# Optimization experiments

Hardware: AMD Instinct MI355X
Metric: run time of the kernel (lower is better)

The kernel has to match this reference:

```python
import jax, jax.numpy as jnp
import numpy as np

B, N, P, DIM, H = 8, 1024, 77, 1024, 16
HD = DIM // H
LN_EPS = 1e-5


def setup_inputs() -> dict:
    key = jax.random.key(0)
    ks = jax.random.split(key, 8)
    s = 0.02  # weight init scale
    return {
        "x": jax.random.normal(ks[0], (B, N, DIM), jnp.float32),
        "x_text": jax.random.normal(ks[1], (B, P, DIM), jnp.float32),
        "Wq": jax.random.normal(ks[2], (DIM, DIM), jnp.float32) * s,
        "Wk": jax.random.normal(ks[3], (DIM, DIM), jnp.float32) * s,
        "Wv": jax.random.normal(ks[4], (DIM, DIM), jnp.float32) * s,
        "gate": jax.random.normal(ks[5], (1, H, 1, 1), jnp.float32) * 0.5,
        "ln_g": jnp.ones((DIM,), jnp.float32),
        "ln_b": jnp.zeros((DIM,), jnp.float32),
        "Wp": jax.random.normal(ks[6], (DIM, DIM), jnp.float32) * s,
        "bp": jnp.zeros((DIM,), jnp.float32),
    }


def reference(x, x_text, Wq, Wk, Wv, gate, ln_g, ln_b, Wp, bp):
    b, n, c = x.shape
    h = gate.shape[1]
    # subln projections; prefix text tokens are concatenated onto k/v (not q)
    q = x @ Wq.T                                             # [B,N,C]
    k = jnp.concatenate([x_text @ Wk.T, x @ Wk.T], axis=1)   # [B,P+N,C]
    v = jnp.concatenate([x_text @ Wv.T, x @ Wv.T], axis=1)   # [B,P+N,C]
    kv = k.shape[1]
    q = q.reshape(b, n, h, -1).transpose(0, 2, 1, 3)         # [B,H,N,d]
    k = k.reshape(b, kv, h, -1).transpose(0, 2, 1, 3)        # [B,H,K,d]
    v = v.reshape(b, kv, h, -1).transpose(0, 2, 1, 3)        # [B,H,K,d]
    d = q.shape[-1]
    scores = jnp.einsum('bhnd,bhkd->bhnk', q, k) / jnp.sqrt(jnp.float32(d))
    # gated split softmax: first key column is softmaxed alone (== 1) and gated
    first = jnp.tanh(gate) * jnp.ones_like(scores[..., :1])  # [B,H,N,1]
    rest = jax.nn.softmax(scores[..., 1:], axis=-1)          # [B,H,N,K-1]
    attn = jnp.concatenate([first, rest], axis=-1)           # [B,H,N,K]
    out = jnp.einsum('bhnk,bhkd->bhnd', attn, v)             # AV reduce
    out = out.transpose(0, 2, 1, 3).reshape(b, n, -1)        # [B,N,C]
    # original casts to bfloat16 then back to LN weight dtype
    out = out.astype(jnp.bfloat16).astype(jnp.float32)
    mu = jnp.mean(out, axis=-1, keepdims=True)
    var = jnp.var(out, axis=-1, keepdims=True)
    out = (out - mu) / jnp.sqrt(var + LN_EPS) * ln_g + ln_b
    return out @ Wp.T + bp
```

## Files before the change

kernel.cpp:

```cpp
#include <hip/hip_runtime.h>
#include <stdint.h>

#define DIM   1024
#define NB    8
#define NSEQ  1024
#define NP    77
#define NH    16
#define NKVR  1104
#define KVP   1104
#define NTILE 18
#define PLD   68
#define QSCALE 0.18033688011112042f

typedef short          bf16x8 __attribute__((ext_vector_type(8)));
typedef float          f32x4  __attribute__((ext_vector_type(4)));
typedef unsigned short u16x8  __attribute__((ext_vector_type(8)));
typedef unsigned short u16x4  __attribute__((ext_vector_type(4)));
typedef unsigned int   u32x4  __attribute__((ext_vector_type(4)));

__device__ __forceinline__ float bf2f(unsigned short h) {
  return __uint_as_float(((unsigned int)h) << 16);
}
__device__ __forceinline__ unsigned short f2bf(float f) {
  unsigned int u = __float_as_uint(f);
  unsigned int r = u + 0x7FFFu + ((u >> 16) & 1u);
  return (unsigned short)(r >> 16);
}
__device__ __forceinline__ unsigned int cvt_pk_bf16(float lo, float hi) {
  unsigned int r;
  asm volatile("v_cvt_pk_bf16_f32 %0, %1, %2" : "=v"(r) : "v"(lo), "v"(hi));
  return r;
}

__global__ __launch_bounds__(256) void cast_kernel(const float* __restrict__ in,
                                                   unsigned short* __restrict__ out,
                                                   int n4, float scale) {
  int i = blockIdx.x * 256 + threadIdx.x;
  if (i >= n4) return;
  float4 v = reinterpret_cast<const float4*>(in)[i];
  u16x4 o;
  o[0] = f2bf(v.x * scale); o[1] = f2bf(v.y * scale);
  o[2] = f2bf(v.z * scale); o[3] = f2bf(v.w * scale);
  reinterpret_cast<u16x4*>(out)[i] = o;
}

__global__ __launch_bounds__(256) void cast_x_kernel(const float* __restrict__ in,
                                                     unsigned short* __restrict__ xkv) {
  int i = blockIdx.x * 256 + threadIdx.x;
  if (i >= (NB * NSEQ * DIM) / 4) return;
  const int e    = i * 4;
  const int row  = e >> 10;
  const int cin  = e & 1023;
  const int batch = row >> 10;
  const int r     = row & 1023;
  float4 v = *reinterpret_cast<const float4*>(in + (size_t)e);
  u16x4 o;
  o[0] = f2bf(v.x); o[1] = f2bf(v.y); o[2] = f2bf(v.z); o[3] = f2bf(v.w);
  *reinterpret_cast<u16x4*>(xkv + (size_t)(batch * NKVR + 80 + r) * DIM + cin) = o;
}

__global__ __launch_bounds__(256) void cast_xt_kernel(const float* __restrict__ in,
                                                      unsigned short* __restrict__ xkv) {
  int i = blockIdx.x * 256 + threadIdx.x;
  if (i >= (NB * NP * DIM) / 4) return;
  const int e    = i * 4;
  const int row  = e >> 10;
  const int cin  = e & 1023;
  const int batch = row / NP;
  const int r     = row - batch * NP;
  float4 v = *reinterpret_cast<const float4*>(in + (size_t)e);
  u16x4 o;
  o[0] = f2bf(v.x); o[1] = f2bf(v.y); o[2] = f2bf(v.z); o[3] = f2bf(v.w);
  *reinterpret_cast<u16x4*>(xkv + (size_t)(batch * NKVR + r) * DIM + cin) = o;
}

__global__ __launch_bounds__(256) void zero_hole_kernel(unsigned short* __restrict__ xkv) {
  int i = blockIdx.x * 256 + threadIdx.x;
  if (i >= (NB * 3 * DIM) / 4) return;
  const int e    = i * 4;
  const int row  = e >> 10;
  const int cin  = e & 1023;
  const int batch = row / 3;
  const int hr    = row - batch * 3;
  u16x4 z = {0, 0, 0, 0};
  *reinterpret_cast<u16x4*>(xkv + (size_t)(batch * NKVR + 77 + hr) * DIM + cin) = z;
}

__device__ __forceinline__ void gload_lds16(const void* g, void* l) {
  __builtin_amdgcn_global_load_lds(
      (const __attribute__((address_space(1))) void*)g,
      (__attribute__((address_space(3))) void*)l, 16, 0, 0);
}

__global__ __launch_bounds__(256) void gemm_qkv(
    const unsigned short* __restrict__ A, const unsigned short* __restrict__ B,
    unsigned short* __restrict__ Qo, unsigned short* __restrict__ Ko,
    unsigned short* __restrict__ Vto) {
  __shared__ __align__(16) unsigned short As[128 * 32];
  __shared__ __align__(16) unsigned short Bs[128 * 32];
  const int id   = blockIdx.x;
  const int sid  = (id & 7) * 207 + (id >> 3);
  const int bx   = sid / 24;
  const int by   = sid - bx * 24;
  const int m0   = bx * 128;
  const int n0   = by * 128;
  const int t    = threadIdx.x;
  const int w    = t >> 6;
  const int lane = t & 63;
  const int wr   = w >> 1, wc = w & 1;
  const int lr   = lane & 15;
  const int k0   = (lane >> 4) * 8;

  f32x4 acc[4][4];
#pragma unroll
  for (int i = 0; i < 4; ++i)
#pragma unroll
    for (int j = 0; j < 4; ++j) acc[i][j] = f32x4{0.f, 0.f, 0.f, 0.f};

  for (int kt = 0; kt < 32; ++kt) {
#pragma unroll
    for (int p = 0; p < 2; ++p) {
      const int c   = p * 256 + t;
      const int row = c >> 2;
      const int cid = c & 3;
      gload_lds16(A + (size_t)(m0 + row) * DIM + kt * 32 + cid * 8,
                  (char*)As + p * 4096 + w * 1024);
      gload_lds16(B + (size_t)(n0 + row) * DIM + kt * 32 + cid * 8,
                  (char*)Bs + p * 4096 + w * 1024);
    }
    __syncthreads();
    bf16x8 af[4], bfr[4];
#pragma unroll
    for (int mi = 0; mi < 4; ++mi)
      af[mi] = *reinterpret_cast<const bf16x8*>(As + (wr * 64 + mi * 16 + lr) * 32 + k0);
#pragma unroll
    for (int ni = 0; ni < 4; ++ni)
      bfr[ni] = *reinterpret_cast<const bf16x8*>(Bs + (wc * 64 + ni * 16 + lr) * 32 + k0);
#pragma unroll
    for (int mi = 0; mi < 4; ++mi)
#pragma unroll
      for (int ni = 0; ni < 4; ++ni)
        acc[mi][ni] = __builtin_amdgcn_mfma_f32_16x16x32_bf16(af[mi], bfr[ni], acc[mi][ni], 0, 0, 0);
    __syncthreads();
  }

  const int rq  = lane >> 4;
  const int seg = n0 >> 10;
  if (seg == 0) {
#pragma unroll
    for (int mi = 0; mi < 4; ++mi) {
#pragma unroll
      for (int i = 0; i < 4; ++i) {
        const int m     = m0 + wr * 64 + mi * 16 + rq * 4 + i;
        const int batch = m / NKVR;
        const int kv    = m - batch * NKVR;
        if (kv < 80) continue;
        const size_t qrow = (size_t)batch * NSEQ + (kv - 80);
#pragma unroll
        for (int ni = 0; ni < 4; ++ni) {
          const int col = n0 + wc * 64 + ni * 16 + lr;
          Qo[qrow * DIM + col] = f2bf(acc[mi][ni][i]);
        }
      }
    }
  } else if (seg == 1) {
#pragma unroll
    for (int mi = 0; mi < 4; ++mi) {
#pragma unroll
      for (int i = 0; i < 4; ++i) {
        const int m = m0 + wr * 64 + mi * 16 + rq * 4 + i;
#pragma unroll
        for (int ni = 0; ni < 4; ++ni) {
          const int col = n0 + wc * 64 + ni * 16 + lr - 1024;
          Ko[(size_t)m * DIM + col] = f2bf(acc[mi][ni][i]);
        }
      }
    }
  } else {
#pragma unroll
    for (int mi = 0; mi < 4; ++mi) {
      const int mb    = m0 + wr * 64 + mi * 16 + rq * 4;
      const int batch = mb / NKVR;
      const int kv    = mb - batch * NKVR;
#pragma unroll
      for (int ni = 0; ni < 4; ++ni) {
        const int col = n0 + wc * 64 + ni * 16 + lr - 2048;
        const int hh = col >> 6, dd = col & 63;
        u16x4 o;
        o[0] = f2bf(acc[mi][ni][0]); o[1] = f2bf(acc[mi][ni][1]);
        o[2] = f2bf(acc[mi][ni][2]); o[3] = f2bf(acc[mi][ni][3]);
        *reinterpret_cast<u16x4*>(Vto +
            ((size_t)((batch * NH + hh) * 64 + dd)) * KVP + kv) = o;
      }
    }
  }
}

__global__ __launch_bounds__(256) void gemm_out(
    const unsigned short* __restrict__ A, const unsigned short* __restrict__ B,
    float* __restrict__ C, const float* __restrict__ bias) {
  __shared__ __align__(16) unsigned short As[128 * 32];
  __shared__ __align__(16) unsigned short Bs[128 * 32];
  const int t    = threadIdx.x;
  const int w    = t >> 6;
  const int lane = t & 63;
  const int m0   = blockIdx.x * 128;
  const int n0   = blockIdx.y * 128;
  const int wr   = w >> 1, wc = w & 1;
  const int lr   = lane & 15;
  const int k0   = (lane >> 4) * 8;

  f32x4 acc[4][4];
#pragma unroll
  for (int i = 0; i < 4; ++i)
#pragma unroll
    for (int j = 0; j < 4; ++j) acc[i][j] = f32x4{0.f, 0.f, 0.f, 0.f};

  for (int kt = 0; kt < 32; ++kt) {
#pragma unroll
    for (int p = 0; p < 2; ++p) {
      const int c   = p * 256 + t;
      const int row = c >> 2;
      const int cid = c & 3;
      gload_lds16(A + (size_t)(m0 + row) * DIM + kt * 32 + cid * 8,
                  (char*)As + p * 4096 + w * 1024);
      gload_lds16(B + (size_t)(n0 + row) * DIM + kt * 32 + cid * 8,
                  (char*)Bs + p * 4096 + w * 1024);
    }
    __syncthreads();
    bf16x8 af[4], bfr[4];
#pragma unroll
    for (int mi = 0; mi < 4; ++mi)
      af[mi] = *reinterpret_cast<const bf16x8*>(As + (wr * 64 + mi * 16 + lr) * 32 + k0);
#pragma unroll
    for (int ni = 0; ni < 4; ++ni)
      bfr[ni] = *reinterpret_cast<const bf16x8*>(Bs + (wc * 64 + ni * 16 + lr) * 32 + k0);
#pragma unroll
    for (int mi = 0; mi < 4; ++mi)
#pragma unroll
      for (int ni = 0; ni < 4; ++ni)
        acc[mi][ni] = __builtin_amdgcn_mfma_f32_16x16x32_bf16(af[mi], bfr[ni], acc[mi][ni], 0, 0, 0);
    __syncthreads();
  }

  const int rq = lane >> 4;
#pragma unroll
  for (int mi = 0; mi < 4; ++mi) {
#pragma unroll
    for (int i = 0; i < 4; ++i) {
      const int m = m0 + wr * 64 + mi * 16 + rq * 4 + i;
#pragma unroll
      for (int ni = 0; ni < 4; ++ni) {
        const int col = n0 + wc * 64 + ni * 16 + lr;
        C[(size_t)m * DIM + col] = acc[mi][ni][i] + bias[col];
      }
    }
  }
}

__global__ __launch_bounds__(128) void attn_mfma(
    const unsigned short* __restrict__ Q, const unsigned short* __restrict__ K,
    const unsigned short* __restrict__ Vt, const float* __restrict__ gate,
    unsigned short* __restrict__ O) {
  const int wid  = threadIdx.x >> 6;
  const int lane = threadIdx.x & 63;
  const int lr   = lane & 15;
  const int lg   = lane >> 4;
  const int bh   = blockIdx.x;
  const int b    = bh >> 4;
  const int h    = bh & 15;
  const int q0   = blockIdx.y * 64 + wid * 32;

  __shared__ __align__(16) float p_lds[2][32 * PLD];

  bf16x8 aq[2][2];
#pragma unroll
  for (int mi = 0; mi < 2; ++mi)
#pragma unroll
    for (int kf = 0; kf < 2; ++kf)
      aq[mi][kf] = *reinterpret_cast<const bf16x8*>(
          Q + ((size_t)(b * NSEQ + q0 + mi * 16 + lr)) * DIM + h * 64 + kf * 32 + lg * 8);

  f32x4 accO[2][4];
#pragma unroll
  for (int mi = 0; mi < 2; ++mi)
#pragma unroll
    for (int n = 0; n < 4; ++n) accO[mi][n] = f32x4{0.f, 0.f, 0.f, 0.f};
  float lsum[2][4];
#pragma unroll
  for (int mi = 0; mi < 2; ++mi)
#pragma unroll
    for (int r = 0; r < 4; ++r) lsum[mi][r] = 0.f;

  const unsigned short* Kbase  = K  + ((size_t)b * NKVR) * DIM + h * 64 + lg * 8;
  const unsigned short* Vtbase = Vt + ((size_t)((b * NH + h) * 64)) * KVP;
  float* pl = p_lds[wid];

  for (int tkv = 0; tkv < NTILE; ++tkv) {
    const int kv0 = tkv * 64;
    bf16x8 bk[4][2];
#pragma unroll
    for (int ni = 0; ni < 4; ++ni) {
      int kvn = kv0 + ni * 16 + lr;
      kvn = kvn < (NKVR - 1) ? kvn : (NKVR - 1);
      const unsigned short* kr = Kbase + (size_t)kvn * DIM;
#pragma unroll
      for (int kf = 0; kf < 2; ++kf)
        bk[ni][kf] = *reinterpret_cast<const bf16x8*>(kr + kf * 32);
    }
    f32x4 S[2][4];
#pragma unroll
    for (int mi = 0; mi < 2; ++mi)
#pragma unroll
      for (int ni = 0; ni < 4; ++ni) S[mi][ni] = f32x4{0.f, 0.f, 0.f, 0.f};
#pragma unroll
    for (int ni = 0; ni < 4; ++ni)
#pragma unroll
      for (int kf = 0; kf < 2; ++kf)
#pragma unroll
        for (int mi = 0; mi < 2; ++mi)
          S[mi][ni] = __builtin_amdgcn_mfma_f32_16x16x32_bf16(aq[mi][kf], bk[ni][kf], S[mi][ni], 0, 0, 0);
    bf16x8 bv[4][2];
#pragma unroll
    for (int n = 0; n < 4; ++n) {
      const unsigned short* vr = Vtbase + (size_t)(n * 16 + lr) * KVP;
#pragma unroll
      for (int kf = 0; kf < 2; ++kf) {
        int kvb = kv0 + kf * 32 + lg * 8;
        kvb = kvb < (KVP - 8) ? kvb : (KVP - 8);
        bv[n][kf] = *reinterpret_cast<const bf16x8*>(vr + kvb);
      }
    }
    if (tkv < 2 || tkv == NTILE - 1) {
#pragma unroll
      for (int ni = 0; ni < 4; ++ni) {
        const int gk = kv0 + ni * 16 + lr;
        const bool bad = (gk == 0) || ((unsigned)(gk - 77) < 3u) || (gk >= NKVR);
        if (bad) {
#pragma unroll
          for (int mi = 0; mi < 2; ++mi)
#pragma unroll
            for (int r = 0; r < 4; ++r) S[mi][ni][r] = -1.0e30f;
        }
      }
    }
#pragma unroll
    for (int mi = 0; mi < 2; ++mi) {
#pragma unroll
      for (int ni = 0; ni < 4; ++ni) {
#pragma unroll
        for (int r = 0; r < 4; ++r)
          S[mi][ni][r] = __builtin_exp2f(S[mi][ni][r]);
      }
#pragma unroll
      for (int r = 0; r < 4; ++r)
        lsum[mi][r] += (S[mi][0][r] + S[mi][1][r]) + (S[mi][2][r] + S[mi][3][r]);
#pragma unroll
      for (int ni = 0; ni < 4; ++ni) {
        float* pw = pl + (size_t)(mi * 16 + lg * 4) * PLD + ni * 16 + lr;
        pw[0 * PLD] = S[mi][ni][0];
        pw[1 * PLD] = S[mi][ni][1];
        pw[2 * PLD] = S[mi][ni][2];
        pw[3 * PLD] = S[mi][ni][3];
      }
    }
    bf16x8 pa[2][2];
#pragma unroll
    for (int mi = 0; mi < 2; ++mi) {
#pragma unroll
      for (int kf = 0; kf < 2; ++kf) {
        const float* pr = pl + (size_t)(mi * 16 + lr) * PLD + kf * 32 + lg * 8;
        const float4 pa0 = *reinterpret_cast<const float4*>(pr);
        const float4 pa1 = *reinterpret_cast<const float4*>(pr + 4);
        u32x4 pk;
        pk[0] = cvt_pk_bf16(pa0.x, pa0.y);
        pk[1] = cvt_pk_bf16(pa0.z, pa0.w);
        pk[2] = cvt_pk_bf16(pa1.x, pa1.y);
        pk[3] = cvt_pk_bf16(pa1.z, pa1.w);
        pa[mi][kf] = __builtin_bit_cast(bf16x8, pk);
      }
    }
#pragma unroll
    for (int n = 0; n < 4; ++n)
#pragma unroll
      for (int kf = 0; kf < 2; ++kf)
#pragma unroll
        for (int mi = 0; mi < 2; ++mi)
          accO[mi][n] = __builtin_amdgcn_mfma_f32_16x16x32_bf16(pa[mi][kf], bv[n][kf], accO[mi][n], 0, 0, 0);
  }

#pragma unroll
  for (int mi = 0; mi < 2; ++mi) {
#pragma unroll
    for (int r = 0; r < 4; ++r) {
      float s = lsum[mi][r];
      s += __shfl_xor(s, 1);
      s += __shfl_xor(s, 2);
      s += __shfl_xor(s, 4);
      s += __shfl_xor(s, 8);
      lsum[mi][r] = 1.f / s;
    }
  }
  const float gv = tanhf(gate[h]);
#pragma unroll
  for (int mi = 0; mi < 2; ++mi) {
#pragma unroll
    for (int n = 0; n < 4; ++n) {
      const float v0 = bf2f(Vtbase[(size_t)(n * 16 + lr) * KVP]);
#pragma unroll
      for (int r = 0; r < 4; ++r) {
        const float o = accO[mi][n][r] * lsum[mi][r] + gv * v0;
        const int q = q0 + mi * 16 + lg * 4 + r;
        O[((size_t)(b * NSEQ + q)) * DIM + h * 64 + n * 16 + lr] = f2bf(o);
      }
    }
  }
}

__global__ __launch_bounds__(256) void ln_kernel(const unsigned short* __restrict__ in,
                                                 const float* __restrict__ g,
                                                 const float* __restrict__ beta,
                                                 unsigned short* __restrict__ out) {
  const int row = blockIdx.x;
  const int t   = threadIdx.x;
  const u16x4 hv = *reinterpret_cast<const u16x4*>(in + (size_t)row * DIM + t * 4);
  const float v0 = bf2f(hv[0]), v1 = bf2f(hv[1]), v2 = bf2f(hv[2]), v3 = bf2f(hv[3]);
  float sum = v0 + v1 + v2 + v3;
  float sq  = v0 * v0 + v1 * v1 + v2 * v2 + v3 * v3;
  for (int off = 32; off; off >>= 1) {
    sum += __shfl_xor(sum, off);
    sq  += __shfl_xor(sq, off);
  }
  __shared__ float red[8];
  if ((t & 63) == 0) { red[t >> 6] = sum; red[4 + (t >> 6)] = sq; }
  __syncthreads();
  sum = red[0] + red[1] + red[2] + red[3];
  sq  = red[4] + red[5] + red[6] + red[7];
  const float mu  = sum * (1.f / DIM);
  const float var = sq * (1.f / DIM) - mu * mu;
  const float rs  = 1.f / sqrtf(var + 1e-5f);
  const float4 gv = *reinterpret_cast<const float4*>(g + t * 4);
  const float4 bv = *reinterpret_cast<const float4*>(beta + t * 4);
  u16x4 o;
  o[0] = f2bf((v0 - mu) * rs * gv.x + bv.x);
  o[1] = f2bf((v1 - mu) * rs * gv.y + bv.y);
  o[2] = f2bf((v2 - mu) * rs * gv.z + bv.z);
  o[3] = f2bf((v3 - mu) * rs * gv.w + bv.w);
  *reinterpret_cast<u16x4*>(out + (size_t)row * DIM + t * 4) = o;
}

extern "C" void kernel_launch(void* const* d_in, const int* in_sizes, int n_in,
                              void* d_out, int out_size, void* d_ws, size_t ws_size,
                              hipStream_t stream) {
  const float* x    = (const float*)d_in[0];
  const float* xt   = (const float*)d_in[1];
  const float* Wq   = (const float*)d_in[2];
  const float* Wk   = (const float*)d_in[3];
  const float* Wv   = (const float*)d_in[4];
  const float* gate = (const float*)d_in[5];
  const float* lng  = (const float*)d_in[6];
  const float* lnbt = (const float*)d_in[7];
  const float* Wp   = (const float*)d_in[8];
  const float* bp   = (const float*)d_in[9];

  char* ws = (char*)d_ws;
  unsigned short* xkvb = (unsigned short*)(ws + 0);
  unsigned short* Wqkv = (unsigned short*)(ws + 18087936);
  unsigned short* Qb   = (unsigned short*)(ws + 24379392);
  unsigned short* Kb   = (unsigned short*)(ws + 41156608);
  unsigned short* Vtb  = (unsigned short*)(ws + 59244544);
  unsigned short* attnb = xkvb;
  unsigned short* lnob  = Qb;
  unsigned short* Wpb   = Wqkv;

  cast_x_kernel<<<dim3((NB * NSEQ * DIM / 4 + 255) / 256), 256, 0, stream>>>(x, xkvb);
  cast_xt_kernel<<<dim3((NB * NP * DIM / 4 + 255) / 256), 256, 0, stream>>>(xt, xkvb);
  zero_hole_kernel<<<dim3((NB * 3 * DIM / 4 + 255) / 256), 256, 0, stream>>>(xkvb);
  const int w4 = DIM * DIM / 4;
  cast_kernel<<<dim3((w4 + 255) / 256), 256, 0, stream>>>(Wq, Wqkv, w4, QSCALE);
  cast_kernel<<<dim3((w4 + 255) / 256), 256, 0, stream>>>(Wk, Wqkv + DIM * DIM, w4, 1.0f);
  cast_kernel<<<dim3((w4 + 255) / 256), 256, 0, stream>>>(Wv, Wqkv + 2 * DIM * DIM, w4, 1.0f);

  gemm_qkv<<<dim3(69 * 24), 256, 0, stream>>>(xkvb, Wqkv, Qb, Kb, Vtb);

  attn_mfma<<<dim3(128, 16), 128, 0, stream>>>(Qb, Kb, Vtb, gate, attnb);

  cast_kernel<<<dim3((w4 + 255) / 256), 256, 0, stream>>>(Wp, Wpb, w4, 1.0f);
  ln_kernel<<<dim3(NB * NSEQ), 256, 0, stream>>>(attnb, lng, lnbt, lnob);
  gemm_out<<<dim3(64, 8), 256, 0, stream>>>(lnob, Wpb, (float*)d_out, bp);
}
```

Baseline: 249.4 us.

## Rewrite attention with 32x32 MFMA transposed scores and register-only P handoff

```diff
diff --git a/kernel.cpp b/kernel.cpp
--- a/kernel.cpp
+++ b/kernel.cpp
@@ -8,12 +8,11 @@
 #define NH    16
 #define NKVR  1104
 #define KVP   1104
-#define NTILE 18
-#define PLD   68
 #define QSCALE 0.18033688011112042f
 
 typedef short          bf16x8 __attribute__((ext_vector_type(8)));
 typedef float          f32x4  __attribute__((ext_vector_type(4)));
+typedef float          f32x16 __attribute__((ext_vector_type(16)));
 typedef unsigned short u16x8  __attribute__((ext_vector_type(8)));
 typedef unsigned short u16x4  __attribute__((ext_vector_type(4)));
 typedef unsigned int   u32x4  __attribute__((ext_vector_type(4)));
@@ -258,161 +257,133 @@
   }
 }
 
-__global__ __launch_bounds__(128) void attn_mfma(
+__global__ __launch_bounds__(128, 4) void attn_mfma(
     const unsigned short* __restrict__ Q, const unsigned short* __restrict__ K,
     const unsigned short* __restrict__ Vt, const float* __restrict__ gate,
     unsigned short* __restrict__ O) {
   const int wid  = threadIdx.x >> 6;
   const int lane = threadIdx.x & 63;
-  const int lr   = lane & 15;
-  const int lg   = lane >> 4;
+  const int ql   = lane & 31;
+  const int hi   = lane >> 5;
   const int bh   = blockIdx.x;
   const int b    = bh >> 4;
   const int h    = bh & 15;
   const int q0   = blockIdx.y * 64 + wid * 32;
 
-  __shared__ __align__(16) float p_lds[2][32 * PLD];
-
-  bf16x8 aq[2][2];
-#pragma unroll
-  for (int mi = 0; mi < 2; ++mi)
-#pragma unroll
-    for (int kf = 0; kf < 2; ++kf)
-      aq[mi][kf] = *reinterpret_cast<const bf16x8*>(
-          Q + ((size_t)(b * NSEQ + q0 + mi * 16 + lr)) * DIM + h * 64 + kf * 32 + lg * 8);
-
-  f32x4 accO[2][4];
-#pragma unroll
-  for (int mi = 0; mi < 2; ++mi)
-#pragma unroll
-    for (int n = 0; n < 4; ++n) accO[mi][n] = f32x4{0.f, 0.f, 0.f, 0.f};
-  float lsum[2][4];
-#pragma unroll
-  for (int mi = 0; mi < 2; ++mi)
-#pragma unroll
-    for (int r = 0; r < 4; ++r) lsum[mi][r] = 0.f;
-
-  const unsigned short* Kbase  = K  + ((size_t)b * NKVR) * DIM + h * 64 + lg * 8;
+  __shared__ float v0f[2][64];
+
   const unsigned short* Vtbase = Vt + ((size_t)((b * NH + h) * 64)) * KVP;
-  float* pl = p_lds[wid];
-
-  for (int tkv = 0; tkv < NTILE; ++tkv) {
-    const int kv0 = tkv * 64;
-    bf16x8 bk[4][2];
-#pragma unroll
-    for (int ni = 0; ni < 4; ++ni) {
-      int kvn = kv0 + ni * 16 + lr;
-      kvn = kvn < (NKVR - 1) ? kvn : (NKVR - 1);
-      const unsigned short* kr = Kbase + (size_t)kvn * DIM;
-#pragma unroll
-      for (int kf = 0; kf < 2; ++kf)
-        bk[ni][kf] = *reinterpret_cast<const bf16x8*>(kr + kf * 32);
-    }
-    f32x4 S[2][4];
-#pragma unroll
-    for (int mi = 0; mi < 2; ++mi)
-#pragma unroll
-      for (int ni = 0; ni < 4; ++ni) S[mi][ni] = f32x4{0.f, 0.f, 0.f, 0.f};
-#pragma unroll
-    for (int ni = 0; ni < 4; ++ni)
-#pragma unroll
-      for (int kf = 0; kf < 2; ++kf)
-#pragma unroll
-        for (int mi = 0; mi < 2; ++mi)
-          S[mi][ni] = __builtin_amdgcn_mfma_f32_16x16x32_bf16(aq[mi][kf], bk[ni][kf], S[mi][ni], 0, 0, 0);
-    bf16x8 bv[4][2];
-#pragma unroll
-    for (int n = 0; n < 4; ++n) {
-      const unsigned short* vr = Vtbase + (size_t)(n * 16 + lr) * KVP;
-#pragma unroll
-      for (int kf = 0; kf < 2; ++kf) {
-        int kvb = kv0 + kf * 32 + lg * 8;
-        kvb = kvb < (KVP - 8) ? kvb : (KVP - 8);
-        bv[n][kf] = *reinterpret_cast<const bf16x8*>(vr + kvb);
+  const unsigned short* Kbase  = K  + ((size_t)b * NKVR) * DIM + h * 64 + hi * 8;
+
+  v0f[wid][lane] = bf2f(Vtbase[(size_t)lane * KVP]);
+
+  bf16x8 bq[4];
+  const unsigned short* Qrow = Q + ((size_t)(b * NSEQ + q0 + ql)) * DIM + h * 64 + hi * 8;
+#pragma unroll
+  for (int j = 0; j < 4; ++j)
+    bq[j] = *reinterpret_cast<const bf16x8*>(Qrow + j * 16);
+
+  f32x16 o0, o1;
+#pragma unroll
+  for (int r = 0; r < 16; ++r) { o0[r] = 0.f; o1[r] = 0.f; }
+  float lsum = 0.f;
+
+  auto kblock = [&](int kbase, int mm) {
+    int krow = kbase + ql;
+    if (mm == 3) krow = krow < NKVR ? krow : (NKVR - 1);
+    const unsigned short* kr = Kbase + (size_t)krow * DIM;
+    bf16x8 ak[4];
+#pragma unroll
+    for (int j = 0; j < 4; ++j)
+      ak[j] = *reinterpret_cast<const bf16x8*>(kr + j * 16);
+
+    f32x16 s;
+#pragma unroll
+    for (int r = 0; r < 16; ++r) s[r] = 0.f;
+#pragma unroll
+    for (int j = 0; j < 4; ++j)
+      s = __builtin_amdgcn_mfma_f32_32x32x16_bf16(ak[j], bq[j], s, 0, 0, 0);
+
+    bf16x8 av[2][2];
+#pragma unroll
+    for (int ss = 0; ss < 2; ++ss) {
+      if (mm == 3 && ss == 1) continue;
+      const int kv = kbase + ss * 16 + hi * 8;
+#pragma unroll
+      for (int n = 0; n < 2; ++n)
+        av[ss][n] = *reinterpret_cast<const bf16x8*>(
+            Vtbase + (size_t)(n * 32 + ql) * KVP + kv);
+    }
+
+    if (mm == 1) {
+      if (hi == 0) s[0] = -1.0e30f;
+    } else if (mm == 2) {
+      if (hi == 1) { s[5] = -1.0e30f; s[6] = -1.0e30f; s[7] = -1.0e30f; }
+    } else if (mm == 3) {
+#pragma unroll
+      for (int r = 8; r < 16; ++r) s[r] = -1.0e30f;
+    }
+
+    float ts = 0.f;
+#pragma unroll
+    for (int r = 0; r < 16; ++r) { s[r] = __builtin_exp2f(s[r]); ts += s[r]; }
+    lsum += ts;
+
+#pragma unroll
+    for (int ss = 0; ss < 2; ++ss) {
+      if (mm == 3 && ss == 1) continue;
+      const int R = 8 * ss;
+      const unsigned int p0 = cvt_pk_bf16(s[R + 0], s[R + 1]);
+      const unsigned int p1 = cvt_pk_bf16(s[R + 2], s[R + 3]);
+      const unsigned int p2 = cvt_pk_bf16(s[R + 4], s[R + 5]);
+      const unsigned int p3 = cvt_pk_bf16(s[R + 6], s[R + 7]);
+      const unsigned int t0 = (unsigned int)__shfl_xor((int)p0, 32);
+      const unsigned int t1 = (unsigned int)__shfl_xor((int)p1, 32);
+      const unsigned int t2 = (unsigned int)__shfl_xor((int)p2, 32);
+      const unsigned int t3 = (unsigned int)__shfl_xor((int)p3, 32);
+      u32x4 wv;
+      wv[0] = hi ? t2 : p0;
+      wv[1] = hi ? t3 : p1;
+      wv[2] = hi ? p2 : t0;
+      wv[3] = hi ? p3 : t1;
+      const bf16x8 bp = __builtin_bit_cast(bf16x8, wv);
+      o0 = __builtin_amdgcn_mfma_f32_32x32x16_bf16(av[ss][0], bp, o0, 0, 0, 0);
+      o1 = __builtin_amdgcn_mfma_f32_32x32x16_bf16(av[ss][1], bp, o1, 0, 0, 0);
+    }
+  };
+
+  kblock(0, 1);
+  kblock(32, 0);
+  kblock(64, 2);
+  kblock(96, 0);
+  for (int t = 2; t < 17; ++t) {
+    kblock(t * 64, 0);
+    kblock(t * 64 + 32, 0);
+  }
+  kblock(1088, 3);
+
+  const float lt  = lsum + __shfl_xor(lsum, 32);
+  const float inv = 1.f / lt;
+  const float gv  = tanhf(gate[h]);
+  unsigned short* Orow = O + ((size_t)(b * NSEQ + q0 + ql)) * DIM + h * 64;
+#pragma unroll
+  for (int n = 0; n < 2; ++n) {
+#pragma unroll
+    for (int g = 0; g < 4; ++g) {
+      const int d0 = n * 32 + 8 * g + 4 * hi;
+      const float4 vv = *reinterpret_cast<const float4*>(&v0f[wid][d0]);
+      float e0, e1, e2, e3;
+      if (n == 0) {
+        e0 = o0[4 * g + 0]; e1 = o0[4 * g + 1]; e2 = o0[4 * g + 2]; e3 = o0[4 * g + 3];
+      } else {
+        e0 = o1[4 * g + 0]; e1 = o1[4 * g + 1]; e2 = o1[4 * g + 2]; e3 = o1[4 * g + 3];
       }
-    }
-    if (tkv < 2 || tkv == NTILE - 1) {
-#pragma unroll
-      for (int ni = 0; ni < 4; ++ni) {
-        const int gk = kv0 + ni * 16 + lr;
-        const bool bad = (gk == 0) || ((unsigned)(gk - 77) < 3u) || (gk >= NKVR);
-        if (bad) {
-#pragma unroll
-          for (int mi = 0; mi < 2; ++mi)
-#pragma unroll
-            for (int r = 0; r < 4; ++r) S[mi][ni][r] = -1.0e30f;
-        }
-      }
-    }
-#pragma unroll
-    for (int mi = 0; mi < 2; ++mi) {
-#pragma unroll
-      for (int ni = 0; ni < 4; ++ni) {
-#pragma unroll
-        for (int r = 0; r < 4; ++r)
-          S[mi][ni][r] = __builtin_exp2f(S[mi][ni][r]);
-      }
-#pragma unroll
-      for (int r = 0; r < 4; ++r)
-        lsum[mi][r] += (S[mi][0][r] + S[mi][1][r]) + (S[mi][2][r] + S[mi][3][r]);
-#pragma unroll
-      for (int ni = 0; ni < 4; ++ni) {
-        float* pw = pl + (size_t)(mi * 16 + lg * 4) * PLD + ni * 16 + lr;
-        pw[0 * PLD] = S[mi][ni][0];
-        pw[1 * PLD] = S[mi][ni][1];
-        pw[2 * PLD] = S[mi][ni][2];
-        pw[3 * PLD] = S[mi][ni][3];
-      }
-    }
-    bf16x8 pa[2][2];
-#pragma unroll
-    for (int mi = 0; mi < 2; ++mi) {
-#pragma unroll
-      for (int kf = 0; kf < 2; ++kf) {
-        const float* pr = pl + (size_t)(mi * 16 + lr) * PLD + kf * 32 + lg * 8;
-        const float4 pa0 = *reinterpret_cast<const float4*>(pr);
-        const float4 pa1 = *reinterpret_cast<const float4*>(pr + 4);
-        u32x4 pk;
-        pk[0] = cvt_pk_bf16(pa0.x, pa0.y);
-        pk[1] = cvt_pk_bf16(pa0.z, pa0.w);
-        pk[2] = cvt_pk_bf16(pa1.x, pa1.y);
-        pk[3] = cvt_pk_bf16(pa1.z, pa1.w);
-        pa[mi][kf] = __builtin_bit_cast(bf16x8, pk);
-      }
-    }
-#pragma unroll
-    for (int n = 0; n < 4; ++n)
-#pragma unroll
-      for (int kf = 0; kf < 2; ++kf)
-#pragma unroll
-        for (int mi = 0; mi < 2; ++mi)
-          accO[mi][n] = __builtin_amdgcn_mfma_f32_16x16x32_bf16(pa[mi][kf], bv[n][kf], accO[mi][n], 0, 0, 0);
-  }
-
-#pragma unroll
-  for (int mi = 0; mi < 2; ++mi) {
-#pragma unroll
-    for (int r = 0; r < 4; ++r) {
-      float s = lsum[mi][r];
-      s += __shfl_xor(s, 1);
-      s += __shfl_xor(s, 2);
-      s += __shfl_xor(s, 4);
-      s += __shfl_xor(s, 8);
-      lsum[mi][r] = 1.f / s;
-    }
-  }
-  const float gv = tanhf(gate[h]);
-#pragma unroll
-  for (int mi = 0; mi < 2; ++mi) {
-#pragma unroll
-    for (int n = 0; n < 4; ++n) {
-      const float v0 = bf2f(Vtbase[(size_t)(n * 16 + lr) * KVP]);
-#pragma unroll
-      for (int r = 0; r < 4; ++r) {
-        const float o = accO[mi][n][r] * lsum[mi][r] + gv * v0;
-        const int q = q0 + mi * 16 + lg * 4 + r;
-        O[((size_t)(b * NSEQ + q)) * DIM + h * 64 + n * 16 + lr] = f2bf(o);
-      }
+      u16x4 ov;
+      ov[0] = f2bf(e0 * inv + gv * vv.x);
+      ov[1] = f2bf(e1 * inv + gv * vv.y);
+      ov[2] = f2bf(e2 * inv + gv * vv.z);
+      ov[3] = f2bf(e3 * inv + gv * vv.w);
+      *reinterpret_cast<u16x4*>(Orow + d0) = ov;
     }
   }
 }
```

Measured after the change: 260.5 us. 1.04x slower.
